# Optimization experiments

Hardware: AMD Instinct MI355X
Metric: run time of the kernel (lower is better)

The kernel has to match this reference:

```python
import jax, jax.numpy as jnp
import numpy as np

N_NODES = 50000
NEG_SLOPE = 0.2  # PyG GATConv default leaky_relu slope


def setup_inputs() -> dict:
    key = jax.random.key(0)
    ks = jax.random.split(key, 12)
    N, E, D_IN, H = N_NODES, 1200000, 128, 64
    sd_in = 1.0 / np.sqrt(D_IN)
    sd_h = 1.0 / np.sqrt(H)
    return {
        "x": jax.random.normal(ks[0], (N, D_IN), jnp.float32),
        "src": jax.random.randint(ks[1], (E,), 0, N, jnp.int32),
        "dst": jax.random.randint(ks[2], (E,), 0, N, jnp.int32),
        "W1_src": jax.random.normal(ks[3], (D_IN, H), jnp.float32) * sd_in,
        "W1_dst": jax.random.normal(ks[4], (D_IN, H), jnp.float32) * sd_in,
        "a1_src": jax.random.normal(ks[5], (H,), jnp.float32) * sd_h,
        "a1_dst": jax.random.normal(ks[6], (H,), jnp.float32) * sd_h,
        "b1": jnp.zeros((H,), jnp.float32),
        "W2_src": jax.random.normal(ks[7], (H, H), jnp.float32) * sd_h,
        "W2_dst": jax.random.normal(ks[8], (H, H), jnp.float32) * sd_h,
        "a2_src": jax.random.normal(ks[9], (H,), jnp.float32) * sd_h,
        "a2_dst": jax.random.normal(ks[10], (H,), jnp.float32) * sd_h,
        "b2": jnp.zeros((H,), jnp.float32),
    }


def _gat_layer(x, src, dst, W_src, W_dst, att_src, att_dst, bias):
    N = x.shape[0]
    h_src = x @ W_src            # [N, H] transformed source features
    h_dst = x @ W_dst            # [N, H] transformed destination features
    alpha_src = h_src @ att_src  # [N]
    alpha_dst = h_dst @ att_dst  # [N]
    # edge-wise attention logits (gather), edge j -> i: e = lrelu(a_src[j] + a_dst[i])
    e = jax.nn.leaky_relu(alpha_src[src] + alpha_dst[dst], NEG_SLOPE)  # [E]
    # segment softmax over incoming edges of each destination node
    m = jax.ops.segment_max(e, dst, num_segments=N)          # [N]
    ex = jnp.exp(e - m[dst])                                  # [E]
    denom = jax.ops.segment_sum(ex, dst, num_segments=N)     # [N]
    alpha = ex / denom[dst]                                   # [E]
    # weighted scatter-add aggregation
    msgs = h_src[src] * alpha[:, None]                        # [E, H]
    out = jax.ops.segment_sum(msgs, dst, num_segments=N)     # [N, H]
    return out + bias


def reference(x, src, dst, W1_src, W1_dst, a1_src, a1_dst, b1,
              W2_src, W2_dst, a2_src, a2_dst, b2):
    h = jnp.tanh(_gat_layer(x, src, dst, W1_src, W1_dst, a1_src, a1_dst, b1))
    h = jnp.tanh(_gat_layer(h, src, dst, W2_src, W2_dst, a2_src, a2_dst, b2))
    return h
```

## Files before the change

kernel.cpp:

```cpp
#include <hip/hip_runtime.h>
#include <hip/hip_bf16.h>

#define NEG_SLOPE 0.2f
#define EPB 4096
#define NHB 64

typedef __attribute__((ext_vector_type(8))) short short8v;
typedef __attribute__((ext_vector_type(4))) float f32x4;

__device__ inline float blo(unsigned u) { return __uint_as_float(u << 16); }
__device__ inline float bhi(unsigned u) { return __uint_as_float(u & 0xffff0000u); }
__device__ inline unsigned short bf16bits(float f) {
    __hip_bfloat16 b = __float2bfloat16(f);
    return *(unsigned short*)&b;
}
__device__ inline unsigned pack2bf(float e, float o) {
    return ((unsigned)bf16bits(o) << 16) | (unsigned)bf16bits(e);
}

template <int K>
__device__ inline void build_wt(unsigned short* __restrict__ Wt,
                                const float* __restrict__ W_src,
                                const float* __restrict__ a_src,
                                const float* __restrict__ W_dst,
                                const float* __restrict__ a_dst, int tid) {
    for (int i = tid; i < 64 * K; i += 256) {
        int k = i >> 6, j = i & 63;
        Wt[j * K + k] = bf16bits(W_src[i]);
    }
    for (int i = tid; i < 2 * K; i += 256) {
        int which = (i >= K) ? 1 : 0;
        int k = i - which * K;
        const float* Wr = (which ? W_dst : W_src) + k * 64;
        const float* av = which ? a_dst : a_src;
        float s = 0.f;
        #pragma unroll
        for (int j = 0; j < 64; ++j) s += Wr[j] * av[j];
        Wt[(64 + which) * K + k] = bf16bits(s);
    }
    for (int i = tid; i < 14 * K; i += 256) Wt[66 * K + i] = 0;
}

__global__ __launch_bounds__(256) void prep(
    const int* __restrict__ dst, int* __restrict__ partials, int E,
    const float* __restrict__ W1_src, const float* __restrict__ a1_src,
    const float* __restrict__ W1_dst, const float* __restrict__ a1_dst,
    const float* __restrict__ W2_src, const float* __restrict__ a2_src,
    const float* __restrict__ W2_dst, const float* __restrict__ a2_dst,
    unsigned short* __restrict__ Wt1, unsigned short* __restrict__ Wt2,
    int* __restrict__ cursor0) {
    __shared__ int lh[256];
    int tid = threadIdx.x, b = blockIdx.x;
    if (b < NHB) {
        lh[tid] = 0;
        __syncthreads();
        for (int e = b * 256 + tid; e < E; e += NHB * 256)
            atomicAdd(&lh[dst[e] >> 8], 1);
        __syncthreads();
        partials[b * 256 + tid] = lh[tid];
    } else if (b == NHB) {
        build_wt<128>(Wt1, W1_src, a1_src, W1_dst, a1_dst, tid);
    } else if (b == NHB + 1) {
        build_wt<64>(Wt2, W2_src, a2_src, W2_dst, a2_dst, tid);
    } else {
        cursor0[tid] = 0;
    }
}

__device__ inline void local_scan(const int* __restrict__ partials,
                                  int* sBase, int* sCnt, int tid) {
    int v = 0;
    #pragma unroll
    for (int b = 0; b < NHB; ++b) v += partials[b * 256 + tid];
    sCnt[tid] = v;
    sBase[tid] = v;
    __syncthreads();
    for (int off = 1; off < 256; off <<= 1) {
        int t = (tid >= off) ? sBase[tid - off] : 0;
        __syncthreads();
        sBase[tid] += t;
        __syncthreads();
    }
    sBase[tid] -= v;
    __syncthreads();
}

template <int K, bool INBF16>
__device__ inline void nt_body(int nb, const void* __restrict__ x_,
                               const unsigned short* __restrict__ Wt,
                               unsigned* __restrict__ hb_out,
                               float* __restrict__ alpha_src,
                               float* __restrict__ alpha_dst, int N, int tid) {
    int wid = tid >> 6, l = tid & 63;
    int rowbase = (nb * 4 + wid) * 16;
    if (rowbase >= N) return;
    int jcol = l & 15, kg = (l >> 4) * 8;

    int r = rowbase + jcol;
    if (r >= N) r = N - 1;
    const float*          xr32 = (const float*)x_ + (size_t)r * K + kg;
    const unsigned short* xr16 = (const unsigned short*)x_ + (size_t)r * K + kg;

    f32x4 acc[5];
    #pragma unroll
    for (int t = 0; t < 5; ++t) acc[t] = (f32x4){0.f, 0.f, 0.f, 0.f};

    #pragma unroll
    for (int kt = 0; kt < K / 32; ++kt) {
        short8v a;
        if constexpr (INBF16) {
            a = *(const short8v*)(xr16 + kt * 32);
        } else {
            float4 xa = *(const float4*)(xr32 + kt * 32);
            float4 xb = *(const float4*)(xr32 + kt * 32 + 4);
            a[0] = (short)bf16bits(xa.x); a[1] = (short)bf16bits(xa.y);
            a[2] = (short)bf16bits(xa.z); a[3] = (short)bf16bits(xa.w);
            a[4] = (short)bf16bits(xb.x); a[5] = (short)bf16bits(xb.y);
            a[6] = (short)bf16bits(xb.z); a[7] = (short)bf16bits(xb.w);
        }
        int kbase = kt * 32 + kg;
        #pragma unroll
        for (int t = 0; t < 5; ++t) {
            short8v b = *(const short8v*)&Wt[(t * 16 + jcol) * K + kbase];
            acc[t] = __builtin_amdgcn_mfma_f32_16x16x32_bf16(a, b, acc[t], 0, 0, 0);
        }
    }

    int rbase = rowbase + (l >> 4) * 4;
    #pragma unroll
    for (int t = 0; t < 4; ++t) {
        #pragma unroll
        for (int rr = 0; rr < 4; ++rr) {
            float v = acc[t][rr];
            float w = __shfl_xor(v, 1);
            int row = rbase + rr;
            if (!(l & 1) && row < N)
                hb_out[(size_t)row * 32 + t * 8 + (jcol >> 1)] = pack2bf(v, w);
        }
    }
    #pragma unroll
    for (int rr = 0; rr < 4; ++rr) {
        int row = rbase + rr;
        if (row < N) {
            if (jcol == 0) alpha_src[row] = acc[4][rr];
            if (jcol == 1) alpha_dst[row] = acc[4][rr];
        }
    }
}

__global__ __launch_bounds__(256) void scatter_nt1(
    const int* __restrict__ src, const int* __restrict__ dst,
    const int* __restrict__ partials, int* __restrict__ cursor0,
    unsigned* __restrict__ ebuf, int E, int eb3,
    const float* __restrict__ x, const unsigned short* __restrict__ Wt1,
    unsigned* __restrict__ hb_out,
    float* __restrict__ alpha_src, float* __restrict__ alpha_dst, int N) {
    int tid = threadIdx.x;
    if ((int)blockIdx.x >= eb3) {
        nt_body<128, false>(blockIdx.x - eb3, x, Wt1, hb_out,
                            alpha_src, alpha_dst, N, tid);
        return;
    }
    __shared__ int sBase[256];
    __shared__ int sCnt[256];
    __shared__ int lhist[256];
    __shared__ int lbase[256];
    local_scan(partials, sBase, sCnt, tid);

    lhist[tid] = 0;
    __syncthreads();
    int base = blockIdx.x * EPB;
    int bkt[16], rank[16];
    unsigned pack[16];
    #pragma unroll
    for (int i = 0; i < 16; ++i) {
        int e = base + i * 256 + tid;
        bkt[i] = -1;
        if (e < E) {
            int d = dst[e], s = src[e];
            bkt[i]  = d >> 8;
            pack[i] = ((unsigned)(d & 255) << 16) | (unsigned)s;
            rank[i] = atomicAdd(&lhist[bkt[i]], 1);
        }
    }
    __syncthreads();
    int cnt = lhist[tid];
    if (cnt) lbase[tid] = sBase[tid] + atomicAdd(&cursor0[tid], cnt);
    __syncthreads();
    #pragma unroll
    for (int i = 0; i < 16; ++i)
        if (bkt[i] >= 0) ebuf[lbase[bkt[i]] + rank[i]] = pack[i];
}

__global__ __launch_bounds__(256) void bucket_build(
    const unsigned* __restrict__ ebuf, const int* __restrict__ partials,
    int* __restrict__ row_ptr, unsigned short* __restrict__ csr16,
    int N, int E) {
    __shared__ int sBase[256];
    __shared__ int sCnt[256];
    __shared__ int deg[256];
    __shared__ int cur[256];
    __shared__ int tmp[256];
    int b = blockIdx.x, tid = threadIdx.x;
    local_scan(partials, sBase, sCnt, tid);
    int ebase = sBase[b], eend = sBase[b] + sCnt[b];

    deg[tid] = 0;
    __syncthreads();
    for (int e = ebase + tid; e < eend; e += 256)
        atomicAdd(&deg[ebuf[e] >> 16], 1);
    __syncthreads();
    int v = deg[tid];
    tmp[tid] = v;
    __syncthreads();
    for (int off = 1; off < 256; off <<= 1) {
        int t = (tid >= off) ? tmp[tid - off] : 0;
        __syncthreads();
        tmp[tid] += t;
        __syncthreads();
    }
    int excl = tmp[tid] - v;
    int node = b * 256 + tid;
    if (node < N) row_ptr[node] = ebase + excl;
    if (b == 0 && tid == 0) row_ptr[N] = E;
    cur[tid] = excl;
    __syncthreads();
    for (int e = ebase + tid; e < eend; e += 256) {
        unsigned pk = ebuf[e];
        int r = atomicAdd(&cur[pk >> 16], 1);
        csr16[ebase + r] = (unsigned short)(pk & 0xFFFFu);
    }
}

template <bool OUTBF16>
__global__ __launch_bounds__(256) void aggregate(
    const int* __restrict__ row_ptr, const unsigned short* __restrict__ csr16,
    const float* __restrict__ alpha_src, const float* __restrict__ alpha_dst,
    const unsigned* __restrict__ hb,
    const float* __restrict__ bias,
    void* __restrict__ out_,
    int N) {
    __shared__ float2 spbuf[4][64];
    int wid = threadIdx.x >> 6, lane = threadIdx.x & 63;
    int node = blockIdx.x * 4 + wid;
    if (node >= N) return;

    int beg = row_ptr[node], end = row_ptr[node + 1];
    float adst = alpha_dst[node];
    int half = lane >> 5, sub = lane & 31;
    float2* __restrict__ mysp = spbuf[wid];
    int wslot = (lane & 1) * 32 + (lane >> 1);
    int rbase = half * 32;

    float dL = 0.f;
    float aA[4] = {0.f, 0.f, 0.f, 0.f};
    float aB[4] = {0.f, 0.f, 0.f, 0.f};

    for (int c = beg; c < end; c += 64) {
        int cnt = end - c;
        cnt = (cnt < 64) ? cnt : 64;

        int s = 0;
        float p = 0.f;
        if (lane < cnt) {
            s = csr16[c + lane];
            float t = alpha_src[s] + adst;
            t = (t > 0.f) ? t : NEG_SLOPE * t;
            p = __expf(fminf(t, 60.f));
            dL += p;
        }
        mysp[wslot] = make_float2(__int_as_float(s), p);

        for (int j = 0; j < cnt; j += 16) {
            int sl = rbase + (j >> 1);
            float4 q0 = *(const float4*)&mysp[sl];
            float4 q1 = *(const float4*)&mysp[sl + 2];
            float4 q2 = *(const float4*)&mysp[sl + 4];
            float4 q3 = *(const float4*)&mysp[sl + 6];
            int   sv[8] = {__float_as_int(q0.x), __float_as_int(q0.z),
                           __float_as_int(q1.x), __float_as_int(q1.z),
                           __float_as_int(q2.x), __float_as_int(q2.z),
                           __float_as_int(q3.x), __float_as_int(q3.z)};
            float pv[8] = {q0.y, q0.w, q1.y, q1.w, q2.y, q2.w, q3.y, q3.w};
            unsigned uv[8];
            #pragma unroll
            for (int i = 0; i < 8; ++i)
                uv[i] = hb[(size_t)sv[i] * 32 + sub];
            #pragma unroll
            for (int i = 0; i < 8; ++i) {
                aA[i & 3] = fmaf(pv[i], blo(uv[i]), aA[i & 3]);
                aB[i & 3] = fmaf(pv[i], bhi(uv[i]), aB[i & 3]);
            }
        }
    }
    float denom = dL;
    #pragma unroll
    for (int off = 32; off; off >>= 1) denom += __shfl_xor(denom, off);

    float accA = (aA[0] + aA[1]) + (aA[2] + aA[3]);
    float accB = (aB[0] + aB[1]) + (aB[2] + aB[3]);
    accA += __shfl_xor(accA, 32);
    accB += __shfl_xor(accB, 32);
    int srcl = lane >> 1;
    float vA = __shfl(accA, srcl);
    float vB = __shfl(accB, srcl);
    float val = (lane & 1) ? vB : vA;
    float r = (denom > 0.f) ? (val / denom) : 0.f;
    float fv = tanhf(r + bias[lane]);

    if constexpr (OUTBF16) {
        float fw = __shfl_xor(fv, 1);
        if (!(lane & 1))
            ((unsigned*)out_)[(size_t)node * 32 + (lane >> 1)] = pack2bf(fv, fw);
    } else {
        ((float*)out_)[(size_t)node * 64 + lane] = fv;
    }
}

__global__ __launch_bounds__(256) void nt2(
    const unsigned short* __restrict__ x, const unsigned short* __restrict__ Wt,
    unsigned* __restrict__ hb_out,
    float* __restrict__ alpha_src, float* __restrict__ alpha_dst, int N) {
    nt_body<64, true>(blockIdx.x, x, Wt, hb_out, alpha_src, alpha_dst,
                      N, threadIdx.x);
}

extern "C" void kernel_launch(void* const* d_in, const int* in_sizes, int n_in,
                              void* d_out, int out_size, void* d_ws, size_t ws_size,
                              hipStream_t stream) {
    const float* x      = (const float*)d_in[0];
    const int*   src    = (const int*)  d_in[1];
    const int*   dst    = (const int*)  d_in[2];
    const float* W1_src = (const float*)d_in[3];
    const float* W1_dst = (const float*)d_in[4];
    const float* a1_src = (const float*)d_in[5];
    const float* a1_dst = (const float*)d_in[6];
    const float* b1     = (const float*)d_in[7];
    const float* W2_src = (const float*)d_in[8];
    const float* W2_dst = (const float*)d_in[9];
    const float* a2_src = (const float*)d_in[10];
    const float* a2_dst = (const float*)d_in[11];
    const float* b2     = (const float*)d_in[12];
    float* out = (float*)d_out;

    const int N = in_sizes[0] / 128;
    const int E = in_sizes[1];
    const int NB = (N + 255) / 256;

    char* ws = (char*)d_ws;
    size_t off = 0;
    auto alloc = [&](size_t bytes) {
        void* p = ws + off;
        off += (bytes + 255) & ~(size_t)255;
        return p;
    };
    unsigned* hbuf1  = (unsigned*)alloc((size_t)N * 32 * 4);
    unsigned* h1buf  = (unsigned*)alloc((size_t)N * 32 * 4);
    unsigned* hbuf2  = (unsigned*)alloc((size_t)N * 32 * 4);
    float* alpha_s1  = (float*)alloc((size_t)N * 4);
    float* alpha_d1  = (float*)alloc((size_t)N * 4);
    float* alpha_s2  = (float*)alloc((size_t)N * 4);
    float* alpha_d2  = (float*)alloc((size_t)N * 4);
    int*   row_ptr   = (int*)  alloc((size_t)(N + 1) * 4);
    unsigned short* csr16 = (unsigned short*)alloc((size_t)E * 2);
    int*   partials  = (int*)  alloc(NHB * 256 * 4);
    int*   cursor0   = (int*)  alloc(256 * 4);
    unsigned short* Wt1 = (unsigned short*)alloc(80 * 128 * 2);
    unsigned short* Wt2 = (unsigned short*)alloc(80 * 64 * 2);
    unsigned* ebuf   = (unsigned*)alloc((size_t)E * 4);
    (void)ws_size;

    const int eb3  = (E + EPB - 1) / EPB;
    const int nwb  = (N + 3) / 4;
    const int ntb  = (N + 63) / 64;

    prep<<<NHB + 3, 256, 0, stream>>>(dst, partials, E,
                                      W1_src, a1_src, W1_dst, a1_dst,
                                      W2_src, a2_src, W2_dst, a2_dst,
                                      Wt1, Wt2, cursor0);
    scatter_nt1<<<eb3 + ntb, 256, 0, stream>>>(
        src, dst, partials, cursor0, ebuf, E, eb3,
        x, Wt1, hbuf1, alpha_s1, alpha_d1, N);
    bucket_build<<<NB, 256, 0, stream>>>(ebuf, partials, row_ptr, csr16, N, E);
    aggregate<true><<<nwb, 256, 0, stream>>>(row_ptr, csr16, alpha_s1, alpha_d1,
                                             hbuf1, b1, h1buf, N);
    nt2<<<ntb, 256, 0, stream>>>((const unsigned short*)h1buf, Wt2,
                                 hbuf2, alpha_s2, alpha_d2, N);
    aggregate<false><<<nwb, 256, 0, stream>>>(row_ptr, csr16, alpha_s2, alpha_d2,
                                              hbuf2, b2, out, N);
}
```

Measured before the change: 131.3 us.

## Use 1024 finer dst buckets with a standalone scan kernel for CSR build

Bucket edges by dst>>6 (1024 buckets of 64 nodes) instead of dst>>8 (256 buckets), and move the bucket prefix scan into a dedicated single-block kernel. The scatter and bucket_build blocks no longer each redo the 64-way partial reduction and scan. bucket_build gets roughly four times as many blocks with smaller per-block work, which should improve parallelism on the CSR build. The cost is an extra kernel launch and more atomics on cursor0 from the scatter blocks, since each block now touches up to 1024 buckets.

Result: no change. 129.5 us, median of 3 (-1.3%).

```diff
diff --git a/kernel.cpp b/kernel.cpp
--- a/kernel.cpp
+++ b/kernel.cpp
@@ -4,6 +4,7 @@
 #define NEG_SLOPE 0.2f
 #define EPB 4096
 #define NHB 64
+#define NBUK 1024
 
 typedef __attribute__((ext_vector_type(8))) short short8v;
 typedef __attribute__((ext_vector_type(4))) float f32x4;
@@ -47,42 +48,50 @@
     const float* __restrict__ W1_dst, const float* __restrict__ a1_dst,
     const float* __restrict__ W2_src, const float* __restrict__ a2_src,
     const float* __restrict__ W2_dst, const float* __restrict__ a2_dst,
-    unsigned short* __restrict__ Wt1, unsigned short* __restrict__ Wt2,
-    int* __restrict__ cursor0) {
-    __shared__ int lh[256];
+    unsigned short* __restrict__ Wt1, unsigned short* __restrict__ Wt2) {
+    __shared__ int lh[NBUK];
     int tid = threadIdx.x, b = blockIdx.x;
     if (b < NHB) {
-        lh[tid] = 0;
+        for (int s = tid; s < NBUK; s += 256) lh[s] = 0;
         __syncthreads();
         for (int e = b * 256 + tid; e < E; e += NHB * 256)
-            atomicAdd(&lh[dst[e] >> 8], 1);
-        __syncthreads();
-        partials[b * 256 + tid] = lh[tid];
+            atomicAdd(&lh[dst[e] >> 6], 1);
+        __syncthreads();
+        for (int s = tid; s < NBUK; s += 256)
+            partials[b * NBUK + s] = lh[s];
     } else if (b == NHB) {
         build_wt<128>(Wt1, W1_src, a1_src, W1_dst, a1_dst, tid);
-    } else if (b == NHB + 1) {
+    } else {
         build_wt<64>(Wt2, W2_src, a2_src, W2_dst, a2_dst, tid);
-    } else {
-        cursor0[tid] = 0;
-    }
-}
-
-__device__ inline void local_scan(const int* __restrict__ partials,
-                                  int* sBase, int* sCnt, int tid) {
-    int v = 0;
-    #pragma unroll
-    for (int b = 0; b < NHB; ++b) v += partials[b * 256 + tid];
-    sCnt[tid] = v;
-    sBase[tid] = v;
+    }
+}
+
+__global__ __launch_bounds__(256) void scan1024(const int* __restrict__ partials,
+                                                int* __restrict__ bucket_base,
+                                                int* __restrict__ cursor0) {
+    __shared__ int tsum[256];
+    int tid = threadIdx.x;
+    int4 v = make_int4(0, 0, 0, 0);
+    for (int b = 0; b < NHB; ++b) {
+        int4 p = *(const int4*)&partials[b * NBUK + 4 * tid];
+        v.x += p.x; v.y += p.y; v.z += p.z; v.w += p.w;
+    }
+    int t = v.x + v.y + v.z + v.w;
+    tsum[tid] = t;
     __syncthreads();
     for (int off = 1; off < 256; off <<= 1) {
-        int t = (tid >= off) ? sBase[tid - off] : 0;
-        __syncthreads();
-        sBase[tid] += t;
-        __syncthreads();
-    }
-    sBase[tid] -= v;
-    __syncthreads();
+        int u = (tid >= off) ? tsum[tid - off] : 0;
+        __syncthreads();
+        tsum[tid] += u;
+        __syncthreads();
+    }
+    int base = tsum[tid] - t;
+    bucket_base[4 * tid + 0] = base;
+    bucket_base[4 * tid + 1] = base + v.x;
+    bucket_base[4 * tid + 2] = base + v.x + v.y;
+    bucket_base[4 * tid + 3] = base + v.x + v.y + v.z;
+    if (tid == 255) bucket_base[NBUK] = tsum[255];
+    *(int4*)&cursor0[4 * tid] = make_int4(0, 0, 0, 0);
 }
 
 template <int K, bool INBF16>
@@ -150,7 +159,7 @@
 
 __global__ __launch_bounds__(256) void scatter_nt1(
     const int* __restrict__ src, const int* __restrict__ dst,
-    const int* __restrict__ partials, int* __restrict__ cursor0,
+    const int* __restrict__ bucket_base, int* __restrict__ cursor0,
     unsigned* __restrict__ ebuf, int E, int eb3,
     const float* __restrict__ x, const unsigned short* __restrict__ Wt1,
     unsigned* __restrict__ hb_out,
@@ -161,13 +170,9 @@
                             alpha_src, alpha_dst, N, tid);
         return;
     }
-    __shared__ int sBase[256];
-    __shared__ int sCnt[256];
-    __shared__ int lhist[256];
-    __shared__ int lbase[256];
-    local_scan(partials, sBase, sCnt, tid);
-
-    lhist[tid] = 0;
+    __shared__ int lhist[NBUK];
+    __shared__ int lbase[NBUK];
+    for (int s = tid; s < NBUK; s += 256) lhist[s] = 0;
     __syncthreads();
     int base = blockIdx.x * EPB;
     int bkt[16], rank[16];
@@ -178,14 +183,16 @@
         bkt[i] = -1;
         if (e < E) {
             int d = dst[e], s = src[e];
-            bkt[i]  = d >> 8;
-            pack[i] = ((unsigned)(d & 255) << 16) | (unsigned)s;
+            bkt[i]  = d >> 6;
+            pack[i] = ((unsigned)(d & 63) << 16) | (unsigned)s;
             rank[i] = atomicAdd(&lhist[bkt[i]], 1);
         }
     }
     __syncthreads();
-    int cnt = lhist[tid];
-    if (cnt) lbase[tid] = sBase[tid] + atomicAdd(&cursor0[tid], cnt);
+    for (int s = tid; s < NBUK; s += 256) {
+        int c = lhist[s];
+        if (c) lbase[s] = bucket_base[s] + atomicAdd(&cursor0[s], c);
+    }
     __syncthreads();
     #pragma unroll
     for (int i = 0; i < 16; ++i)
@@ -193,37 +200,33 @@
 }
 
 __global__ __launch_bounds__(256) void bucket_build(
-    const unsigned* __restrict__ ebuf, const int* __restrict__ partials,
+    const unsigned* __restrict__ ebuf, const int* __restrict__ bucket_base,
     int* __restrict__ row_ptr, unsigned short* __restrict__ csr16,
     int N, int E) {
-    __shared__ int sBase[256];
-    __shared__ int sCnt[256];
-    __shared__ int deg[256];
-    __shared__ int cur[256];
+    __shared__ int deg[64];
+    __shared__ int cur[64];
     __shared__ int tmp[256];
     int b = blockIdx.x, tid = threadIdx.x;
-    local_scan(partials, sBase, sCnt, tid);
-    int ebase = sBase[b], eend = sBase[b] + sCnt[b];
-
-    deg[tid] = 0;
+    int ebase = bucket_base[b], eend = bucket_base[b + 1];
+    if (tid < 64) deg[tid] = 0;
     __syncthreads();
     for (int e = ebase + tid; e < eend; e += 256)
         atomicAdd(&deg[ebuf[e] >> 16], 1);
     __syncthreads();
-    int v = deg[tid];
+    int v = (tid < 64) ? deg[tid] : 0;
     tmp[tid] = v;
     __syncthreads();
-    for (int off = 1; off < 256; off <<= 1) {
+    for (int off = 1; off < 64; off <<= 1) {
         int t = (tid >= off) ? tmp[tid - off] : 0;
         __syncthreads();
         tmp[tid] += t;
         __syncthreads();
     }
     int excl = tmp[tid] - v;
-    int node = b * 256 + tid;
-    if (node < N) row_ptr[node] = ebase + excl;
+    int node = b * 64 + tid;
+    if (tid < 64 && node < N) row_ptr[node] = ebase + excl;
     if (b == 0 && tid == 0) row_ptr[N] = E;
-    cur[tid] = excl;
+    if (tid < 64) cur[tid] = excl;
     __syncthreads();
     for (int e = ebase + tid; e < eend; e += 256) {
         unsigned pk = ebuf[e];
@@ -345,7 +348,7 @@
 
     const int N = in_sizes[0] / 128;
     const int E = in_sizes[1];
-    const int NB = (N + 255) / 256;
+    const int nbuk = (N + 63) / 64;
 
     char* ws = (char*)d_ws;
     size_t off = 0;
@@ -363,8 +366,9 @@
     float* alpha_d2  = (float*)alloc((size_t)N * 4);
     int*   row_ptr   = (int*)  alloc((size_t)(N + 1) * 4);
     unsigned short* csr16 = (unsigned short*)alloc((size_t)E * 2);
-    int*   partials  = (int*)  alloc(NHB * 256 * 4);
-    int*   cursor0   = (int*)  alloc(256 * 4);
+    int*   partials  = (int*)  alloc((size_t)NHB * NBUK * 4);
+    int*   bucket_base = (int*)alloc((NBUK + 1) * 4);
+    int*   cursor0   = (int*)  alloc(NBUK * 4);
     unsigned short* Wt1 = (unsigned short*)alloc(80 * 128 * 2);
     unsigned short* Wt2 = (unsigned short*)alloc(80 * 64 * 2);
     unsigned* ebuf   = (unsigned*)alloc((size_t)E * 4);
@@ -374,14 +378,15 @@
     const int nwb  = (N + 3) / 4;
     const int ntb  = (N + 63) / 64;
 
-    prep<<<NHB + 3, 256, 0, stream>>>(dst, partials, E,
+    prep<<<NHB + 2, 256, 0, stream>>>(dst, partials, E,
                                       W1_src, a1_src, W1_dst, a1_dst,
                                       W2_src, a2_src, W2_dst, a2_dst,
-                                      Wt1, Wt2, cursor0);
+                                      Wt1, Wt2);
+    scan1024<<<1, 256, 0, stream>>>(partials, bucket_base, cursor0);
     scatter_nt1<<<eb3 + ntb, 256, 0, stream>>>(
-        src, dst, partials, cursor0, ebuf, E, eb3,
+        src, dst, bucket_base, cursor0, ebuf, E, eb3,
         x, Wt1, hbuf1, alpha_s1, alpha_d1, N);
-    bucket_build<<<NB, 256, 0, stream>>>(ebuf, partials, row_ptr, csr16, N, E);
+    bucket_build<<<nbuk, 256, 0, stream>>>(ebuf, bucket_base, row_ptr, csr16, N, E);
     aggregate<true><<<nwb, 256, 0, stream>>>(row_ptr, csr16, alpha_s1, alpha_d1,
                                              hbuf1, b1, h1buf, N);
     nt2<<<ntb, 256, 0, stream>>>((const unsigned short*)h1buf, Wt2,
```
